# Kernel tuning notes

Measured on AMD Instinct MI355X. Metric: run time of the kernel, lower is better.

## Reference

```python
import jax, jax.numpy as jnp
import numpy as np

EPS = 1e-5
NUM_GROUPS = 32


def setup_inputs() -> dict:
    key = jax.random.key(0)
    ks = jax.random.split(key, 4)
    b, c, h, w = 8, 512, 32, 32
    x = jax.random.normal(ks[0], (b, c, h, w), dtype=jnp.float32)
    gn_weight = jnp.ones((c,), dtype=jnp.float32)
    gn_bias = jnp.zeros((c,), dtype=jnp.float32)
    qkv_w = jax.random.normal(ks[1], (3 * c, c), dtype=jnp.float32) * (1.0 / np.sqrt(c))
    qkv_b = jnp.zeros((3 * c,), dtype=jnp.float32)
    proj_w = jax.random.normal(ks[2], (c, c), dtype=jnp.float32) * (1.0 / np.sqrt(c))
    proj_b = jnp.zeros((c,), dtype=jnp.float32)
    return {"x": x, "gn_weight": gn_weight, "gn_bias": gn_bias,
            "qkv_w": qkv_w, "qkv_b": qkv_b, "proj_w": proj_w, "proj_b": proj_b}


def _group_norm(x, weight, bias):
    b, c, h, w = x.shape
    xg = x.reshape(b, NUM_GROUPS, c // NUM_GROUPS, h, w)
    mean = xg.mean(axis=(2, 3, 4), keepdims=True)
    var = xg.var(axis=(2, 3, 4), keepdims=True)
    xn = ((xg - mean) * jax.lax.rsqrt(var + EPS)).reshape(b, c, h, w)
    return xn * weight[None, :, None, None] + bias[None, :, None, None]


def reference(x, gn_weight, gn_bias, qkv_w, qkv_b, proj_w, proj_b):
    b, c, h, w = x.shape
    scale = c ** (-0.5)
    xn = _group_norm(x, gn_weight, gn_bias)
    # 1x1 conv == per-pixel matmul over channels
    qkv = jnp.einsum('bchw,oc->bohw', xn, qkv_w) + qkv_b[None, :, None, None]
    q, k, v = jnp.split(qkv.reshape(b, 3 * c, h * w), 3, axis=1)  # each [b, c, N]
    attn = jax.nn.softmax(jnp.einsum('bci,bcj->bij', q, k) * scale, axis=-1)
    out = jnp.einsum('bij,bcj->bci', attn, v).reshape(b, c, h, w)
    proj = jnp.einsum('bchw,oc->bohw', out, proj_w) + proj_b[None, :, None, None]
    return x + proj
```

## Files before the change

kernel.cpp:

```cpp
#include <hip/hip_runtime.h>
#include <cmath>

constexpr int Bsz = 8, Cch = 512, NPIX = 1024;
constexpr int NG = 32, CPG = 16;

typedef __attribute__((ext_vector_type(4))) float f32x4;
typedef __attribute__((ext_vector_type(8))) short s16x8;

#define GLOBAL_AS __attribute__((address_space(1)))
#define LDS_AS __attribute__((address_space(3)))

__device__ inline short f2bf(float f) {
  union { float f; unsigned u; } c = {f};
  unsigned r = (c.u + 0x7fffu + ((c.u >> 16) & 1u)) >> 16;
  return (short)r;
}

__device__ inline float wave_reduce_sum(float v) {
#pragma unroll
  for (int off = 32; off > 0; off >>= 1) v += __shfl_xor(v, off, 64);
  return v;
}

__global__ __launch_bounds__(256) void prep_kernel(
    const float* __restrict__ x, const float* __restrict__ w,
    const float* __restrict__ bb, short* __restrict__ xnt,
    const float* __restrict__ in1, short* __restrict__ out1, int n1,
    const float* __restrict__ in2, short* __restrict__ out2, int n2,
    float* __restrict__ lsum) {
  __shared__ float sm[8];
  if (blockIdx.x == 1280) {
    float4 z = {0.f, 0.f, 0.f, 0.f};
    float4* p = (float4*)lsum;
#pragma unroll
    for (int i = 0; i < 8; ++i) p[threadIdx.x + i * 256] = z;
    return;
  }
  if (blockIdx.x >= 256) {
    const int i = ((blockIdx.x - 256) * 256 + threadIdx.x) * 4;
    const float* in = in1;
    short* out = out1;
    int j = i;
    if (i >= n1) { in = in2; out = out2; j = i - n1; }
    if (j + 3 < (i >= n1 ? n2 : n1)) {
      float4 v = *(const float4*)(in + j);
      short o[4] = {f2bf(v.x), f2bf(v.y), f2bf(v.z), f2bf(v.w)};
      *(uint2*)(out + j) = *(const uint2*)o;
    }
    return;
  }
  const int bg = blockIdx.x, b = bg >> 5, g = bg & 31;
  const float* xp = x + ((size_t)(b * Cch + g * CPG)) * NPIX;
  float s = 0.f, ss = 0.f;
  for (int i = threadIdx.x * 4; i < CPG * NPIX; i += 1024) {
    float4 v = *(const float4*)(xp + i);
    s += v.x + v.y + v.z + v.w;
    ss += v.x * v.x + v.y * v.y + v.z * v.z + v.w * v.w;
  }
  s = wave_reduce_sum(s);
  ss = wave_reduce_sum(ss);
  const int wv = threadIdx.x >> 6;
  if ((threadIdx.x & 63) == 0) { sm[wv] = s; sm[4 + wv] = ss; }
  __syncthreads();
  const float tsum = sm[0] + sm[1] + sm[2] + sm[3];
  const float tsq = sm[4] + sm[5] + sm[6] + sm[7];
  const float inv_n = 1.0f / (CPG * NPIX);
  const float mean = tsum * inv_n;
  const float rstd = rsqrtf(tsq * inv_n - mean * mean + 1e-5f);
  float wc[CPG], bc[CPG];
#pragma unroll
  for (int c = 0; c < CPG; ++c) {
    wc[c] = w[g * CPG + c] * rstd;
    bc[c] = bb[g * CPG + c] - mean * wc[c];
  }
  const int p0 = threadIdx.x * 4;
  short ov[4][CPG];
#pragma unroll
  for (int c = 0; c < CPG; ++c) {
    float4 v = *(const float4*)(xp + (size_t)c * NPIX + p0);
    ov[0][c] = f2bf(v.x * wc[c] + bc[c]);
    ov[1][c] = f2bf(v.y * wc[c] + bc[c]);
    ov[2][c] = f2bf(v.z * wc[c] + bc[c]);
    ov[3][c] = f2bf(v.w * wc[c] + bc[c]);
  }
#pragma unroll
  for (int j = 0; j < 4; ++j) {
    short* op = xnt + ((size_t)(b * NPIX + p0 + j)) * Cch + g * CPG;
    *(uint4*)op = *(const uint4*)&ov[j][0];
    *(uint4*)(op + 8) = *(const uint4*)&ov[j][8];
  }
}

template <int BM, int BN, int EPI>
__global__ __launch_bounds__(256) void mfma_gemm(
    const short* __restrict__ A, const short* __restrict__ B, int K, int lda,
    int ldb, long sA, long sB, const float* __restrict__ bias, float alpha,
    void* __restrict__ Cp, long sC, int ldc, void* __restrict__ C2p, long sC2,
    const float* __restrict__ resid, long sR) {
  constexpr int FM = BM / 32, FN = BN / 32;
  constexpr int NA = BM / 64, NB = BN / 64;
  __shared__ __align__(16) short Asl[BM * 32];
  __shared__ __align__(16) short Bsl[BN * 32];
  const int t = threadIdx.x;
  const int lane = t & 63, wave = t >> 6;

  const int gx = gridDim.x, gy = gridDim.y;
  const int nwg = gx * gy * (int)gridDim.z;
  int flat = (int)blockIdx.x + gx * ((int)blockIdx.y + gy * (int)blockIdx.z);
  flat = (flat & 7) * (nwg >> 3) + (flat >> 3);
  const int bx = flat % gx;
  const int rem = flat / gx;
  const int by = rem % gy;
  const int bz = rem / gy;

  const int m0 = by * BM, n0 = bx * BN;
  A += sA * bz;
  B += sB * bz;

  const short* ga[NA];
  const short* gb[NB];
  short* la[NA];
  short* lb[NB];
#pragma unroll
  for (int i = 0; i < NA; ++i) {
    const int s = i * 256 + t;
    const int row = ((s >> 6) * 16) + (s & 15);
    const int q = (s >> 4) & 3;
    ga[i] = A + (size_t)(m0 + row) * lda + q * 8;
    la[i] = Asl + s * 8;
  }
#pragma unroll
  for (int i = 0; i < NB; ++i) {
    const int s = i * 256 + t;
    const int row = ((s >> 6) * 16) + (s & 15);
    const int q = (s >> 4) & 3;
    gb[i] = B + (size_t)(n0 + row) * ldb + q * 8;
    lb[i] = Bsl + s * 8;
  }

  f32x4 acc[FM][FN] = {};
  const int wm = wave & 1, wn = wave >> 1;

  for (int k0 = 0; k0 < K; k0 += 32) {
#pragma unroll
    for (int i = 0; i < NA; ++i) {
      __builtin_amdgcn_global_load_lds((const GLOBAL_AS void*)ga[i],
                                       (LDS_AS void*)la[i], 16, 0, 0);
      ga[i] += 32;
    }
#pragma unroll
    for (int i = 0; i < NB; ++i) {
      __builtin_amdgcn_global_load_lds((const GLOBAL_AS void*)gb[i],
                                       (LDS_AS void*)lb[i], 16, 0, 0);
      gb[i] += 32;
    }
    __syncthreads();
    s16x8 af[FM], bf[FN];
#pragma unroll
    for (int i = 0; i < FM; ++i)
      af[i] = *(const s16x8*)(Asl + (wm * FM + i) * 512 + lane * 8);
#pragma unroll
    for (int i = 0; i < FN; ++i)
      bf[i] = *(const s16x8*)(Bsl + (wn * FN + i) * 512 + lane * 8);
#pragma unroll
    for (int im = 0; im < FM; ++im)
#pragma unroll
      for (int in = 0; in < FN; ++in)
        acc[im][in] = __builtin_amdgcn_mfma_f32_16x16x32_bf16(
            af[im], bf[in], acc[im][in], 0, 0, 0);
    __syncthreads();
  }

  const int quad = lane >> 4, nn = lane & 15;
  if (EPI == 1) {
    short* Cs = (short*)Cp + sC * bz;
    float* L = (float*)C2p + sC2 * bz;
#pragma unroll
    for (int im = 0; im < FM; ++im) {
      const int m = m0 + (wm * FM + im) * 16 + quad * 4;
      float rs[4] = {0.f, 0.f, 0.f, 0.f};
#pragma unroll
      for (int in = 0; in < FN; ++in) {
        const int n = n0 + (wn * FN + in) * 16 + nn;
#pragma unroll
        for (int r = 0; r < 4; ++r) {
          const float e = __expf(acc[im][in][r] * alpha);
          rs[r] += e;
          Cs[(size_t)(m + r) * ldc + n] = f2bf(e);
        }
      }
#pragma unroll
      for (int off = 1; off < 16; off <<= 1)
#pragma unroll
        for (int r = 0; r < 4; ++r) rs[r] += __shfl_xor(rs[r], off, 64);
      if (nn == 0) {
#pragma unroll
        for (int r = 0; r < 4; ++r) atomicAdd(&L[m + r], rs[r]);
      }
    }
    return;
  }
#pragma unroll
  for (int im = 0; im < FM; ++im) {
    float invl[4];
    if (EPI == 2) {
      const float* L = resid + sR * bz;
      const int m = m0 + (wm * FM + im) * 16 + quad * 4;
#pragma unroll
      for (int r = 0; r < 4; ++r) invl[r] = 1.0f / L[m + r];
    }
#pragma unroll
    for (int in = 0; in < FN; ++in) {
      const int m = m0 + (wm * FM + im) * 16 + quad * 4;
      const int n = n0 + (wn * FN + in) * 16 + nn;
      if (EPI == 0) {
        if (m0 < 1024) {
          short* Cq = (short*)Cp + sC * bz;
          short o[4];
#pragma unroll
          for (int r = 0; r < 4; ++r) o[r] = f2bf(acc[im][in][r] + bias[m + r]);
          *(uint2*)(Cq + (size_t)n * ldc + m) = *(const uint2*)o;
        } else {
          short* Cv = (short*)C2p + sC2 * bz;
#pragma unroll
          for (int r = 0; r < 4; ++r)
            Cv[(size_t)(m - 1024 + r) * ldc + n] =
                f2bf(acc[im][in][r] + bias[m + r]);
        }
      } else if (EPI == 2) {
        short* Cs = (short*)Cp + sC * bz;
#pragma unroll
        for (int r = 0; r < 4; ++r)
          Cs[(size_t)(m + r) * ldc + n] = f2bf(acc[im][in][r] * invl[r]);
      } else {
        float* Cf = (float*)Cp + sC * bz;
        const float* R = resid + sR * bz;
#pragma unroll
        for (int r = 0; r < 4; ++r)
          Cf[(size_t)(m + r) * ldc + n] =
              acc[im][in][r] + bias[m + r] + R[(size_t)(m + r) * ldc + n];
      }
    }
  }
}

extern "C" void kernel_launch(void* const* d_in, const int* in_sizes, int n_in,
                              void* d_out, int out_size, void* d_ws,
                              size_t ws_size, hipStream_t stream) {
  const float* x = (const float*)d_in[0];
  const float* gnw = (const float*)d_in[1];
  const float* gnb = (const float*)d_in[2];
  const float* qkvw = (const float*)d_in[3];
  const float* qkvb = (const float*)d_in[4];
  const float* projw = (const float*)d_in[5];
  const float* projb = (const float*)d_in[6];
  float* out = (float*)d_out;

  char* ws = (char*)d_ws;
  short* xnt = (short*)ws;
  short* qkt = (short*)(ws + (8ull << 20));
  short* vbuf = (short*)(ws + (24ull << 20));
  short* Pbuf = (short*)(ws + (32ull << 20));
  short* Ot = (short*)(ws + (48ull << 20));
  short* wq = (short*)(ws + (56ull << 20));
  short* wp = (short*)(ws + (58ull << 20));
  float* lsum = (float*)(ws + (60ull << 20));

  prep_kernel<<<1281, 256, 0, stream>>>(x, gnw, gnb, xnt, qkvw, wq, 1536 * 512,
                                        projw, wp, 512 * 512, lsum);

  mfma_gemm<128, 64, 0><<<dim3(16, 12, Bsz), 256, 0, stream>>>(
      wq, xnt, 512, 512, 512, 0L, 1024L * 512, qkvb, 1.0f, qkt, 1024L * 1024,
      1024, vbuf, 512L * 1024, nullptr, 0L);

  const float scale = 1.0f / sqrtf(512.0f);
  mfma_gemm<128, 64, 1><<<dim3(16, 8, Bsz), 256, 0, stream>>>(
      qkt, qkt + 512, 512, 1024, 1024, 1024L * 1024, 1024L * 1024, nullptr,
      scale, Pbuf, 1024L * 1024, 1024, lsum, 1024L, nullptr, 0L);

  mfma_gemm<64, 64, 2><<<dim3(8, 16, Bsz), 256, 0, stream>>>(
      Pbuf, vbuf, 1024, 1024, 1024, 1024L * 1024, 512L * 1024, nullptr, 1.0f,
      Ot, 1024L * 512, 512, nullptr, 0L, lsum, 1024L);

  mfma_gemm<64, 64, 3><<<dim3(16, 8, Bsz), 256, 0, stream>>>(
      wp, Ot, 512, 512, 512, 0L, 1024L * 512, projb, 1.0f, out, 512L * 1024,
      1024, nullptr, 0L, x, 512L * 1024);
}
```

Measured before the change: 221.6 us.

## Triple-buffer GEMM LDS loads with async prefetch and enlarge tile sizes

```diff
diff --git a/kernel.cpp b/kernel.cpp
--- a/kernel.cpp
+++ b/kernel.cpp
@@ -99,8 +99,10 @@
     const float* __restrict__ resid, long sR) {
   constexpr int FM = BM / 32, FN = BN / 32;
   constexpr int NA = BM / 64, NB = BN / 64;
-  __shared__ __align__(16) short Asl[BM * 32];
-  __shared__ __align__(16) short Bsl[BN * 32];
+  constexpr int ASZ = BM * 32, BSZ = BN * 32;
+  constexpr int NBUF = 3;
+  __shared__ __align__(16) short Asl[NBUF * ASZ];
+  __shared__ __align__(16) short Bsl[NBUF * BSZ];
   const int t = threadIdx.x;
   const int lane = t & 63, wave = t >> 6;
 
@@ -138,37 +140,59 @@
     lb[i] = Bsl + s * 8;
   }
 
+  auto stage = [&](int slot) {
+#pragma unroll
+    for (int i = 0; i < NA; ++i) {
+      __builtin_amdgcn_global_load_lds((const GLOBAL_AS void*)ga[i],
+                                       (LDS_AS void*)(la[i] + slot * ASZ), 16,
+                                       0, 0);
+      ga[i] += 32;
+    }
+#pragma unroll
+    for (int i = 0; i < NB; ++i) {
+      __builtin_amdgcn_global_load_lds((const GLOBAL_AS void*)gb[i],
+                                       (LDS_AS void*)(lb[i] + slot * BSZ), 16,
+                                       0, 0);
+      gb[i] += 32;
+    }
+  };
+
   f32x4 acc[FM][FN] = {};
   const int wm = wave & 1, wn = wave >> 1;
-
-  for (int k0 = 0; k0 < K; k0 += 32) {
-#pragma unroll
-    for (int i = 0; i < NA; ++i) {
-      __builtin_amdgcn_global_load_lds((const GLOBAL_AS void*)ga[i],
-                                       (LDS_AS void*)la[i], 16, 0, 0);
-      ga[i] += 32;
-    }
-#pragma unroll
-    for (int i = 0; i < NB; ++i) {
-      __builtin_amdgcn_global_load_lds((const GLOBAL_AS void*)gb[i],
-                                       (LDS_AS void*)lb[i], 16, 0, 0);
-      gb[i] += 32;
-    }
-    __syncthreads();
+  const int NT = K >> 5;
+
+  stage(0);
+  stage(1);
+  int cs = 0, ps = 2;
+  for (int kt = 0; kt < NT; ++kt) {
+    asm volatile("s_barrier" ::: "memory");
+    if (kt + 2 < NT) {
+      stage(ps);
+      asm volatile("s_waitcnt vmcnt(%0)\n\ts_barrier" ::"n"(2 * (NA + NB))
+                   : "memory");
+    } else if (kt + 1 < NT) {
+      asm volatile("s_waitcnt vmcnt(%0)\n\ts_barrier" ::"n"(NA + NB)
+                   : "memory");
+    } else {
+      asm volatile("s_waitcnt vmcnt(0)\n\ts_barrier" ::: "memory");
+    }
+    const short* Ab = Asl + cs * ASZ;
+    const short* Bb = Bsl + cs * BSZ;
     s16x8 af[FM], bf[FN];
 #pragma unroll
     for (int i = 0; i < FM; ++i)
-      af[i] = *(const s16x8*)(Asl + (wm * FM + i) * 512 + lane * 8);
+      af[i] = *(const s16x8*)(Ab + (wm * FM + i) * 512 + lane * 8);
 #pragma unroll
     for (int i = 0; i < FN; ++i)
-      bf[i] = *(const s16x8*)(Bsl + (wn * FN + i) * 512 + lane * 8);
+      bf[i] = *(const s16x8*)(Bb + (wn * FN + i) * 512 + lane * 8);
 #pragma unroll
     for (int im = 0; im < FM; ++im)
 #pragma unroll
       for (int in = 0; in < FN; ++in)
         acc[im][in] = __builtin_amdgcn_mfma_f32_16x16x32_bf16(
             af[im], bf[in], acc[im][in], 0, 0, 0);
-    __syncthreads();
+    cs = (cs + 1 == NBUF) ? 0 : cs + 1;
+    ps = (ps + 1 == NBUF) ? 0 : ps + 1;
   }
 
   const int quad = lane >> 4, nn = lane & 15;
@@ -269,20 +293,20 @@
   prep_kernel<<<1281, 256, 0, stream>>>(x, gnw, gnb, xnt, qkvw, wq, 1536 * 512,
                                         projw, wp, 512 * 512, lsum);
 
-  mfma_gemm<128, 64, 0><<<dim3(16, 12, Bsz), 256, 0, stream>>>(
+  mfma_gemm<128, 128, 0><<<dim3(8, 12, Bsz), 256, 0, stream>>>(
       wq, xnt, 512, 512, 512, 0L, 1024L * 512, qkvb, 1.0f, qkt, 1024L * 1024,
       1024, vbuf, 512L * 1024, nullptr, 0L);
 
   const float scale = 1.0f / sqrtf(512.0f);
-  mfma_gemm<128, 64, 1><<<dim3(16, 8, Bsz), 256, 0, stream>>>(
+  mfma_gemm<128, 128, 1><<<dim3(8, 8, Bsz), 256, 0, stream>>>(
       qkt, qkt + 512, 512, 1024, 1024, 1024L * 1024, 1024L * 1024, nullptr,
       scale, Pbuf, 1024L * 1024, 1024, lsum, 1024L, nullptr, 0L);
 
-  mfma_gemm<64, 64, 2><<<dim3(8, 16, Bsz), 256, 0, stream>>>(
+  mfma_gemm<128, 64, 2><<<dim3(8, 8, Bsz), 256, 0, stream>>>(
       Pbuf, vbuf, 1024, 1024, 1024, 1024L * 1024, 512L * 1024, nullptr, 1.0f,
       Ot, 1024L * 512, 512, nullptr, 0L, lsum, 1024L);
 
-  mfma_gemm<64, 64, 3><<<dim3(16, 8, Bsz), 256, 0, stream>>>(
+  mfma_gemm<64, 128, 3><<<dim3(8, 8, Bsz), 256, 0, stream>>>(
       wp, Ot, 512, 512, 512, 0L, 1024L * 512, projb, 1.0f, out, 512L * 1024,
       1024, nullptr, 0L, x, 512L * 1024);
 }
```

Result: faster. 193.5 us (-12.7%).

## Add double-buffered 256-row GEMM kernel for QKV and scores, retile remaining GEMMs

Applied to the files above, without the earlier changes.

```diff
diff --git a/kernel.cpp b/kernel.cpp
--- a/kernel.cpp
+++ b/kernel.cpp
@@ -49,7 +49,8 @@
     }
     return;
   }
-  const int bg = blockIdx.x, b = bg >> 5, g = bg & 31;
+  const int bg = ((int)blockIdx.x & 7) * 32 + ((int)blockIdx.x >> 3);
+  const int b = bg >> 5, g = bg & 31;
   const float* xp = x + ((size_t)(b * Cch + g * CPG)) * NPIX;
   float s = 0.f, ss = 0.f;
   for (int i = threadIdx.x * 4; i < CPG * NPIX; i += 1024) {
@@ -91,18 +92,21 @@
   }
 }
 
-template <int BM, int BN, int EPI>
-__global__ __launch_bounds__(256) void mfma_gemm(
+template <int BN, int EPI>
+__global__ __launch_bounds__(512, 2) void gemm256(
     const short* __restrict__ A, const short* __restrict__ B, int K, int lda,
     int ldb, long sA, long sB, const float* __restrict__ bias, float alpha,
-    void* __restrict__ Cp, long sC, int ldc, void* __restrict__ C2p, long sC2,
-    const float* __restrict__ resid, long sR) {
-  constexpr int FM = BM / 32, FN = BN / 32;
-  constexpr int NA = BM / 64, NB = BN / 64;
-  __shared__ __align__(16) short Asl[BM * 32];
-  __shared__ __align__(16) short Bsl[BN * 32];
+    void* __restrict__ Cp, long sC, int ldc, void* __restrict__ C2p, long sC2) {
+  constexpr int FN = BN / 64;
+  constexpr int NBI = BN / 128;
+  constexpr int G = 2 + NBI;
+  constexpr int ASZ = 256 * 32;
+  constexpr int BSZ = BN * 32;
+  __shared__ __align__(16) short Asl[2 * ASZ];
+  __shared__ __align__(16) short Bsl[2 * BSZ];
   const int t = threadIdx.x;
   const int lane = t & 63, wave = t >> 6;
+  const int wm = wave >> 2, wn = wave & 3;
 
   const int gx = gridDim.x, gy = gridDim.y;
   const int nwg = gx * gy * (int)gridDim.z;
@@ -113,6 +117,166 @@
   const int by = rem % gy;
   const int bz = rem / gy;
 
+  const int m0 = by * 256, n0 = bx * BN;
+  A += sA * bz;
+  B += sB * bz;
+
+  const short* ga[2];
+  const short* gb[NBI];
+  short* la[2];
+  short* lb[NBI];
+#pragma unroll
+  for (int i = 0; i < 2; ++i) {
+    const int c = i * 512 + t;
+    const int row = ((c >> 6) << 4) + (c & 15);
+    const int q = (c >> 4) & 3;
+    ga[i] = A + (size_t)(m0 + row) * lda + q * 8;
+    la[i] = Asl + c * 8;
+  }
+#pragma unroll
+  for (int i = 0; i < NBI; ++i) {
+    const int c = i * 512 + t;
+    const int row = ((c >> 6) << 4) + (c & 15);
+    const int q = (c >> 4) & 3;
+    gb[i] = B + (size_t)(n0 + row) * ldb + q * 8;
+    lb[i] = Bsl + c * 8;
+  }
+
+  auto stage = [&](int slot) {
+#pragma unroll
+    for (int i = 0; i < 2; ++i) {
+      __builtin_amdgcn_global_load_lds((const GLOBAL_AS void*)ga[i],
+                                       (LDS_AS void*)(la[i] + slot * ASZ), 16,
+                                       0, 0);
+      ga[i] += 32;
+    }
+#pragma unroll
+    for (int i = 0; i < NBI; ++i) {
+      __builtin_amdgcn_global_load_lds((const GLOBAL_AS void*)gb[i],
+                                       (LDS_AS void*)(lb[i] + slot * BSZ), 16,
+                                       0, 0);
+      gb[i] += 32;
+    }
+  };
+
+  f32x4 acc[8][FN] = {};
+  const int NT = K >> 5;
+
+  stage(0);
+  for (int kt = 0; kt < NT; ++kt) {
+    const int cur = kt & 1;
+    if (kt + 1 < NT) {
+      stage(cur ^ 1);
+      asm volatile("s_waitcnt vmcnt(%0)\n\ts_barrier" ::"n"(G) : "memory");
+    } else {
+      asm volatile("s_waitcnt vmcnt(0)\n\ts_barrier" ::: "memory");
+    }
+    const short* Ab = Asl + cur * ASZ;
+    const short* Bb = Bsl + cur * BSZ;
+    s16x8 af[4], bf[FN];
+#pragma unroll
+    for (int j = 0; j < 4; ++j)
+      af[j] = *(const s16x8*)(Ab + (wm * 8 + j) * 512 + lane * 8);
+#pragma unroll
+    for (int in = 0; in < FN; ++in)
+      bf[in] = *(const s16x8*)(Bb + (wn * FN + in) * 512 + lane * 8);
+    __builtin_amdgcn_s_setprio(1);
+#pragma unroll
+    for (int im = 0; im < 4; ++im)
+#pragma unroll
+      for (int in = 0; in < FN; ++in)
+        acc[im][in] = __builtin_amdgcn_mfma_f32_16x16x32_bf16(
+            af[im], bf[in], acc[im][in], 0, 0, 0);
+    __builtin_amdgcn_s_setprio(0);
+    asm volatile("s_waitcnt lgkmcnt(0)\n\ts_barrier" ::: "memory");
+#pragma unroll
+    for (int j = 0; j < 4; ++j)
+      af[j] = *(const s16x8*)(Ab + (wm * 8 + 4 + j) * 512 + lane * 8);
+    __builtin_amdgcn_s_setprio(1);
+#pragma unroll
+    for (int im = 0; im < 4; ++im)
+#pragma unroll
+      for (int in = 0; in < FN; ++in)
+        acc[4 + im][in] = __builtin_amdgcn_mfma_f32_16x16x32_bf16(
+            af[im], bf[in], acc[4 + im][in], 0, 0, 0);
+    __builtin_amdgcn_s_setprio(0);
+    asm volatile("s_waitcnt lgkmcnt(0)\n\ts_barrier" ::: "memory");
+  }
+
+  const int quad = lane >> 4, nn = lane & 15;
+  if (EPI == 1) {
+    short* Cs = (short*)Cp + sC * bz;
+    float* L = (float*)C2p + sC2 * bz;
+#pragma unroll
+    for (int im = 0; im < 8; ++im) {
+      const int m = m0 + wm * 128 + im * 16 + quad * 4;
+      float rs[4] = {0.f, 0.f, 0.f, 0.f};
+#pragma unroll
+      for (int in = 0; in < FN; ++in) {
+        const int n = n0 + wn * (FN * 16) + in * 16 + nn;
+#pragma unroll
+        for (int r = 0; r < 4; ++r) {
+          const float e = __expf(acc[im][in][r] * alpha);
+          rs[r] += e;
+          Cs[(size_t)(m + r) * ldc + n] = f2bf(e);
+        }
+      }
+#pragma unroll
+      for (int off = 1; off < 16; off <<= 1)
+#pragma unroll
+        for (int r = 0; r < 4; ++r) rs[r] += __shfl_xor(rs[r], off, 64);
+      if (nn == 0) {
+#pragma unroll
+        for (int r = 0; r < 4; ++r) atomicAdd(&L[m + r], rs[r]);
+      }
+    }
+    return;
+  }
+#pragma unroll
+  for (int im = 0; im < 8; ++im) {
+#pragma unroll
+    for (int in = 0; in < FN; ++in) {
+      const int m = m0 + wm * 128 + im * 16 + quad * 4;
+      const int n = n0 + wn * (FN * 16) + in * 16 + nn;
+      if (m0 < 1024) {
+        short* Cq = (short*)Cp + sC * bz;
+        short o[4];
+#pragma unroll
+        for (int r = 0; r < 4; ++r) o[r] = f2bf(acc[im][in][r] + bias[m + r]);
+        *(uint2*)(Cq + (size_t)n * ldc + m) = *(const uint2*)o;
+      } else {
+        short* Cv = (short*)C2p + sC2 * bz;
+#pragma unroll
+        for (int r = 0; r < 4; ++r)
+          Cv[(size_t)(m - 1024 + r) * ldc + n] =
+              f2bf(acc[im][in][r] + bias[m + r]);
+      }
+    }
+  }
+}
+
+template <int BM, int BN, int EPI>
+__global__ __launch_bounds__(256) void mfma_gemm(
+    const short* __restrict__ A, const short* __restrict__ B, int K, int lda,
+    int ldb, long sA, long sB, const float* __restrict__ bias, float alpha,
+    void* __restrict__ Cp, long sC, int ldc,
+    const float* __restrict__ resid, long sR) {
+  constexpr int FM = BM / 32, FN = BN / 32;
+  constexpr int NA = BM / 64, NB = BN / 64;
+  __shared__ __align__(16) short Asl[BM * 32];
+  __shared__ __align__(16) short Bsl[BN * 32];
+  const int t = threadIdx.x;
+  const int lane = t & 63, wave = t >> 6;
+
+  const int gx = gridDim.x, gy = gridDim.y;
+  const int nwg = gx * gy * (int)gridDim.z;
+  int flat = (int)blockIdx.x + gx * ((int)blockIdx.y + gy * (int)blockIdx.z);
+  flat = (flat & 7) * (nwg >> 3) + (flat >> 3);
+  const int bx = flat % gx;
+  const int rem = flat / gx;
+  const int by = rem % gy;
+  const int bz = rem / gy;
+
   const int m0 = by * BM, n0 = bx * BN;
   A += sA * bz;
   B += sB * bz;
@@ -172,34 +336,6 @@
   }
 
   const int quad = lane >> 4, nn = lane & 15;
-  if (EPI == 1) {
-    short* Cs = (short*)Cp + sC * bz;
-    float* L = (float*)C2p + sC2 * bz;
-#pragma unroll
-    for (int im = 0; im < FM; ++im) {
-      const int m = m0 + (wm * FM + im) * 16 + quad * 4;
-      float rs[4] = {0.f, 0.f, 0.f, 0.f};
-#pragma unroll
-      for (int in = 0; in < FN; ++in) {
-        const int n = n0 + (wn * FN + in) * 16 + nn;
-#pragma unroll
-        for (int r = 0; r < 4; ++r) {
-          const float e = __expf(acc[im][in][r] * alpha);
-          rs[r] += e;
-          Cs[(size_t)(m + r) * ldc + n] = f2bf(e);
-        }
-      }
-#pragma unroll
-      for (int off = 1; off < 16; off <<= 1)
-#pragma unroll
-        for (int r = 0; r < 4; ++r) rs[r] += __shfl_xor(rs[r], off, 64);
-      if (nn == 0) {
-#pragma unroll
-        for (int r = 0; r < 4; ++r) atomicAdd(&L[m + r], rs[r]);
-      }
-    }
-    return;
-  }
 #pragma unroll
   for (int im = 0; im < FM; ++im) {
     float invl[4];
@@ -213,21 +349,7 @@
     for (int in = 0; in < FN; ++in) {
       const int m = m0 + (wm * FM + im) * 16 + quad * 4;
       const int n = n0 + (wn * FN + in) * 16 + nn;
-      if (EPI == 0) {
-        if (m0 < 1024) {
-          short* Cq = (short*)Cp + sC * bz;
-          short o[4];
-#pragma unroll
-          for (int r = 0; r < 4; ++r) o[r] = f2bf(acc[im][in][r] + bias[m + r]);
-          *(uint2*)(Cq + (size_t)n * ldc + m) = *(const uint2*)o;
-        } else {
-          short* Cv = (short*)C2p + sC2 * bz;
-#pragma unroll
-          for (int r = 0; r < 4; ++r)
-            Cv[(size_t)(m - 1024 + r) * ldc + n] =
-                f2bf(acc[im][in][r] + bias[m + r]);
-        }
-      } else if (EPI == 2) {
+      if (EPI == 2) {
         short* Cs = (short*)Cp + sC * bz;
 #pragma unroll
         for (int r = 0; r < 4; ++r)
@@ -269,20 +391,20 @@
   prep_kernel<<<1281, 256, 0, stream>>>(x, gnw, gnb, xnt, qkvw, wq, 1536 * 512,
                                         projw, wp, 512 * 512, lsum);
 
-  mfma_gemm<128, 64, 0><<<dim3(16, 12, Bsz), 256, 0, stream>>>(
+  gemm256<256, 0><<<dim3(4, 6, Bsz), 512, 0, stream>>>(
       wq, xnt, 512, 512, 512, 0L, 1024L * 512, qkvb, 1.0f, qkt, 1024L * 1024,
-      1024, vbuf, 512L * 1024, nullptr, 0L);
+      1024, vbuf, 512L * 1024);
 
   const float scale = 1.0f / sqrtf(512.0f);
-  mfma_gemm<128, 64, 1><<<dim3(16, 8, Bsz), 256, 0, stream>>>(
+  gemm256<128, 1><<<dim3(8, 4, Bsz), 512, 0, stream>>>(
       qkt, qkt + 512, 512, 1024, 1024, 1024L * 1024, 1024L * 1024, nullptr,
-      scale, Pbuf, 1024L * 1024, 1024, lsum, 1024L, nullptr, 0L);
-
-  mfma_gemm<64, 64, 2><<<dim3(8, 16, Bsz), 256, 0, stream>>>(
+      scale, Pbuf, 1024L * 1024, 1024, lsum, 1024L);
+
+  mfma_gemm<128, 64, 2><<<dim3(8, 8, Bsz), 256, 0, stream>>>(
       Pbuf, vbuf, 1024, 1024, 1024, 1024L * 1024, 512L * 1024, nullptr, 1.0f,
-      Ot, 1024L * 512, 512, nullptr, 0L, lsum, 1024L);
-
-  mfma_gemm<64, 64, 3><<<dim3(16, 8, Bsz), 256, 0, stream>>>(
+      Ot, 1024L * 512, 512, lsum, 1024L);
+
+  mfma_gemm<64, 128, 3><<<dim3(8, 8, Bsz), 256, 0, stream>>>(
       wp, Ot, 512, 512, 512, 0L, 1024L * 512, projb, 1.0f, out, 512L * 1024,
-      1024, nullptr, 0L, x, 512L * 1024);
-}
+      1024, x, 512L * 1024);
+}
```

Result: faster. 201.6 us (-9.0%).
